# Kernel optimization log

Measured on AMD Instinct MI355X. Metric: run time of the kernel, lower is better.

## Reference

```python
import jax, jax.numpy as jnp
import numpy as np
from jax import lax

B, C, H, W = 64, 1, 256, 256
N = H * W
K = 16384  # positive_trials
LOG_CLAMP = -100.0  # torch BCELoss clamps log terms at -100


def setup_inputs() -> dict:
    key = jax.random.key(0)
    k1, k2, k3 = jax.random.split(key, 3)
    decision_scores = jax.random.normal(k1, (B, N, 2), dtype=jnp.float32)
    s_map = jax.random.uniform(k2, (B, C, H, W), dtype=jnp.float32)
    # gumbel noise g = -log(-log(U)), matching F.gumbel_softmax sampling
    u = jax.random.uniform(k3, (B, N, 2), dtype=jnp.float32, minval=1e-10, maxval=1.0)
    gumbel_noise = -jnp.log(-jnp.log(u))
    return {"decision_scores": decision_scores, "s_map": s_map, "gumbel_noise": gumbel_noise}


def reference(decision_scores, s_map, gumbel_noise):
    # Tokenizer: b c h w -> b (h w) c
    tokens = jnp.transpose(s_map.reshape(B, C, H * W), (0, 2, 1))  # [B, N, 1]
    # soft gumbel-softmax (tau=1, hard=False), keep prob of class 0
    soft = jax.nn.softmax(decision_scores + gumbel_noise, axis=-1)[:, :, 0:1]  # [B, N, 1]
    # top-K salient token indices per sample (descending sort -> top_k)
    _, idx = lax.top_k(tokens[:, :, 0], K)  # [B, K]
    trials = jnp.zeros((B, N), dtype=tokens.dtype)
    trials = trials.at[jnp.arange(B)[:, None], idx].set(1.0)[:, :, None]  # [B, N, 1]
    # BCE with reduction='sum', log clamped at -100 like torch
    log_p = jnp.clip(jnp.log(soft), LOG_CLAMP, None)
    log_1mp = jnp.clip(jnp.log(1.0 - soft), LOG_CLAMP, None)
    loss = -jnp.sum(trials * log_p + (1.0 - trials) * log_1mp)
    return loss
```

## Files before the change

### kernel.cpp

```cpp
#include <hip/hip_runtime.h>
#include <cstdint>

#define BATCH 64
#define NPIX 65536
#define TOPK 16384
#define NB 256
#define SEGS 32
#define WLO 186
#define WHI 198
#define NWBIN (WHI - WLO + 1)
#define CAPB 192
#define NSLOT (SEGS * CAPB)
#define FCAP 1024

__device__ __forceinline__ float block_reduce(float acc) {
    __shared__ float w[4];
    __syncthreads();
    #pragma unroll
    for (int off = 32; off > 0; off >>= 1) acc += __shfl_down(acc, off, 64);
    if ((threadIdx.x & 63) == 0) w[threadIdx.x >> 6] = acc;
    __syncthreads();
    return w[0] + w[1] + w[2] + w[3];
}

__device__ __forceinline__ float block_reduce1k(float acc) {
    __shared__ float w[16];
    __syncthreads();
    #pragma unroll
    for (int off = 32; off > 0; off >>= 1) acc += __shfl_down(acc, off, 64);
    if ((threadIdx.x & 63) == 0) w[threadIdx.x >> 6] = acc;
    __syncthreads();
    float s = 0.f;
    #pragma unroll
    for (int i = 0; i < 16; ++i) s += w[i];
    return s;
}

__device__ __forceinline__ void bce_from_d(float d, float& lp, float& llp) {
    float t = __logf(1.f + __expf(-fabsf(d)));
    lp  = fmaxf(fminf(d, 0.f) - t, -100.f);
    llp = fmaxf(-fmaxf(d, 0.f) - t, -100.f);
}

__device__ __forceinline__ int vkey(float v) {
    return (int)fminf(v * 256.0f, 255.0f);
}

__global__ __launch_bounds__(256) void k1_pass(
    const float4* __restrict__ sc, const float4* __restrict__ gn,
    const float2* __restrict__ tokp,
    float* __restrict__ pk1, float* __restrict__ psel, float* __restrict__ phi,
    uint32_t* __restrict__ gcc,
    uint32_t* __restrict__ cvb, uint32_t* __restrict__ cvi,
    uint32_t* __restrict__ cvd, float* __restrict__ out)
{
    __shared__ uint32_t bvb[CAPB], bvi[CAPB], bvd[CAPB];
    __shared__ uint32_t ccount;
    const int tid = threadIdx.x;
    if (tid < CAPB) { bvb[tid] = 0u; bvi[tid] = 0u; bvd[tid] = 0u; }
    if (tid == 0) { ccount = 0u; if (blockIdx.x == 0) out[0] = 0.f; }
    __syncthreads();

    const int b   = blockIdx.x >> 5;
    const int seg = blockIdx.x & (SEGS - 1);
    const int pairbase = b * (NPIX / 2) + seg * 1024;
    float acc = 0.f, asel = 0.f, chi = 0.f;

    #pragma unroll
    for (int it = 0; it < 4; ++it) {
        int j = pairbase + it * 256 + tid;
        float4 s = sc[j];
        float4 g = gn[j];
        float2 tk = tokp[j];
        int px0 = (j - b * (NPIX / 2)) * 2;
        {
            float d = (s.x + g.x) - (s.y + g.y);
            float lp, llp; bce_from_d(d, lp, llp);
            acc += llp;
            float diff = lp - llp;
            int k = vkey(tk.x);
            if (k > WHI) { asel += diff; chi += 1.f; }
            else if (k >= WLO) {
                uint32_t p = atomicAdd(&ccount, 1u);
                if (p < CAPB) {
                    bvb[p] = __float_as_uint(tk.x);
                    bvi[p] = (uint32_t)px0;
                    bvd[p] = __float_as_uint(diff);
                }
            }
        }
        {
            float d = (s.z + g.z) - (s.w + g.w);
            float lp, llp; bce_from_d(d, lp, llp);
            acc += llp;
            float diff = lp - llp;
            int k = vkey(tk.y);
            if (k > WHI) { asel += diff; chi += 1.f; }
            else if (k >= WLO) {
                uint32_t p = atomicAdd(&ccount, 1u);
                if (p < CAPB) {
                    bvb[p] = __float_as_uint(tk.y);
                    bvi[p] = (uint32_t)(px0 + 1);
                    bvd[p] = __float_as_uint(diff);
                }
            }
        }
    }
    __syncthreads();
    const size_t cbase = (size_t)blockIdx.x * CAPB;
    if (tid < CAPB) {
        cvb[cbase + tid] = bvb[tid];
        cvi[cbase + tid] = bvi[tid];
        cvd[cbase + tid] = bvd[tid];
    }
    if (tid == 0) gcc[blockIdx.x] = ccount;

    float t1 = block_reduce(acc);
    float t2 = block_reduce(asel);
    float t3 = block_reduce(chi);
    if (tid == 0) {
        pk1[blockIdx.x]  = t1;
        psel[blockIdx.x] = t2;
        phi[blockIdx.x]  = t3;
    }
}

__global__ __launch_bounds__(1024) void k4_finalize(
    const uint32_t* __restrict__ cvb, const uint32_t* __restrict__ cvi,
    const uint32_t* __restrict__ cvd, const uint32_t* __restrict__ gcc,
    const float* __restrict__ pk1, const float* __restrict__ psel,
    const float* __restrict__ phi,
    const float4* __restrict__ tok4,
    const float2* __restrict__ sc2, const float2* __restrict__ gn2,
    float* __restrict__ out)
{
    __shared__ uint32_t fvb[FCAP], fvi[FCAP];
    __shared__ float    fdf[FCAP];
    __shared__ uint32_t fh[NB];
    __shared__ uint32_t wlds[16 * NWBIN];
    __shared__ uint32_t wc[NWBIN];
    __shared__ uint32_t fcnt;
    __shared__ int      sh_sb, sh_ovf;
    __shared__ uint32_t sh_rem;

    const int b = blockIdx.x, tid = threadIdx.x;
    const int wave = tid >> 6, lane = tid & 63;
    if (tid == 0) { fcnt = 0u; sh_sb = -1; sh_ovf = 0; sh_rem = 1u; }
    __syncthreads();

    const size_t base = (size_t)b * NSLOT;

    int bc[NWBIN];
    #pragma unroll
    for (int i = 0; i < NWBIN; ++i) bc[i] = 0;
    #pragma unroll
    for (int it = 0; it < NSLOT / 1024; ++it) {
        int k = vkey(__uint_as_float(cvb[base + it * 1024 + tid]));
        #pragma unroll
        for (int i = 0; i < NWBIN; ++i) bc[i] += (k == WLO + i);
    }
    #pragma unroll
    for (int i = 0; i < NWBIN; ++i) {
        int v = bc[i];
        #pragma unroll
        for (int off = 32; off > 0; off >>= 1) v += __shfl_down(v, off, 64);
        if (lane == 0) wlds[wave * NWBIN + i] = (uint32_t)v;
    }
    if (tid < SEGS && gcc[b * SEGS + tid] > CAPB) sh_ovf = 1;
    __syncthreads();
    if (tid < NWBIN) {
        uint32_t u = 0;
        #pragma unroll
        for (int wv = 0; wv < 16; ++wv) u += wlds[wv * NWBIN + tid];
        wc[tid] = u;
    }
    float chl = (tid < SEGS) ? phi[b * SEGS + tid] : 0.f;
    float chf = block_reduce1k(chl);
    if (tid == 0) {
        uint32_t cnt_hi = (uint32_t)(chf + 0.5f);
        if (cnt_hi >= TOPK) sh_ovf = 1;
        else {
            uint32_t cum = cnt_hi;
            int found = -1; uint32_t rem = 1u;
            for (int jj = WHI; jj >= WLO; --jj) {
                uint32_t nc = cum + wc[jj - WLO];
                if (nc >= TOPK) { found = jj; rem = TOPK - cum; break; }
                cum = nc;
            }
            if (found < 0) sh_ovf = 1;
            else { sh_sb = found; sh_rem = rem; }
        }
    }
    __syncthreads();

    bool fast = (sh_ovf == 0);
    const int sb = sh_sb;
    float fac = (tid < SEGS) ? pk1[b * SEGS + tid] : 0.f;

    if (fast) {
        if (tid < SEGS) fac += psel[b * SEGS + tid];
        #pragma unroll
        for (int it = 0; it < NSLOT / 1024; ++it) {
            int t = it * 1024 + tid;
            uint32_t vb = cvb[base + t];
            int k = vkey(__uint_as_float(vb));
            if (k > sb) fac += __uint_as_float(cvd[base + t]);
            else if (k == sb) {
                uint32_t p = atomicAdd(&fcnt, 1u);
                if (p < FCAP) {
                    fvb[p] = vb;
                    fvi[p] = cvi[base + t] & (NPIX - 1);
                    fdf[p] = __uint_as_float(cvd[base + t]);
                }
            }
        }
        __syncthreads();
        if (fcnt > FCAP) fast = false;
        if (fast) {
            const uint32_t cnt = fcnt, rem = sh_rem;
            for (uint32_t j = tid; j < cnt; j += 1024) {
                const uint32_t mb = fvb[j], mi = fvi[j];
                uint32_t rank = 0;
                for (uint32_t i = 0; i < cnt; ++i) {
                    uint32_t ob = fvb[i];
                    rank += (ob > mb) || (ob == mb && fvi[i] < mi);
                }
                if (rank < rem) fac += fdf[j];
            }
        }
    }

    if (!fast) {
        fac = (tid < SEGS) ? pk1[b * SEGS + tid] : 0.f;
        for (int i = tid; i < NB; i += 1024) fh[i] = 0u;
        if (tid == 0) fcnt = 0u;
        __syncthreads();
        const float4* tbase = tok4 + (size_t)b * (NPIX / 4);
        for (int it = 0; it < NPIX / 4 / 1024; ++it) {
            float4 v = tbase[it * 1024 + tid];
            atomicAdd(&fh[vkey(v.x)], 1u);
            atomicAdd(&fh[vkey(v.y)], 1u);
            atomicAdd(&fh[vkey(v.z)], 1u);
            atomicAdd(&fh[vkey(v.w)], 1u);
        }
        __syncthreads();
        if (tid == 0) {
            uint32_t cum = 0; int bin = NB - 1;
            for (; bin > 0; --bin) {
                if (cum + fh[bin] >= TOPK) break;
                cum += fh[bin];
            }
            sh_sb = bin; sh_rem = TOPK - cum;
        }
        __syncthreads();
        const int sb2 = sh_sb; const uint32_t rem2 = sh_rem;
        for (int it = 0; it < NPIX / 4 / 1024; ++it) {
            int j = it * 1024 + tid;
            float4 v = tbase[j];
            int px = j * 4;
            float fv[4] = {v.x, v.y, v.z, v.w};
            #pragma unroll
            for (int q = 0; q < 4; ++q) {
                int k = vkey(fv[q]);
                if (k > sb2) {
                    size_t idx = (size_t)b * NPIX + (px + q);
                    float2 S = sc2[idx]; float2 G = gn2[idx];
                    float d = (S.x + G.x) - (S.y + G.y);
                    float lp, llp; bce_from_d(d, lp, llp);
                    fac += lp - llp;
                } else if (k == sb2) {
                    uint32_t p = atomicAdd(&fcnt, 1u);
                    if (p < FCAP) { fvb[p] = __float_as_uint(fv[q]); fvi[p] = (uint32_t)(px + q); }
                }
            }
        }
        __syncthreads();
        const uint32_t cnt2 = min(fcnt, (uint32_t)FCAP);
        for (uint32_t j = tid; j < cnt2; j += 1024) {
            const uint32_t mb = fvb[j], mi = fvi[j];
            uint32_t rank = 0;
            for (uint32_t i = 0; i < cnt2; ++i) {
                uint32_t ob = fvb[i];
                rank += (ob > mb) || (ob == mb && fvi[i] < mi);
            }
            if (rank < rem2) {
                size_t idx = (size_t)b * NPIX + (mi & (NPIX - 1));
                float2 S = sc2[idx]; float2 G = gn2[idx];
                float d = (S.x + G.x) - (S.y + G.y);
                float lp, llp; bce_from_d(d, lp, llp);
                fac += lp - llp;
            }
        }
    }

    float tot = block_reduce1k(fac);
    if (tid == 0) atomicAdd(out, -tot);
}

extern "C" void kernel_launch(void* const* d_in, const int* in_sizes, int n_in,
                              void* d_out, int out_size, void* d_ws, size_t ws_size,
                              hipStream_t stream) {
    const float* scores = (const float*)d_in[0];
    const float* smap   = (const float*)d_in[1];
    const float* gumbel = (const float*)d_in[2];
    float* out = (float*)d_out;

    char* ws = (char*)d_ws;
    float*    pk1  = (float*)ws;     ws += (size_t)BATCH * SEGS * 4;
    float*    psel = (float*)ws;     ws += (size_t)BATCH * SEGS * 4;
    float*    phi  = (float*)ws;     ws += (size_t)BATCH * SEGS * 4;
    uint32_t* gcc  = (uint32_t*)ws;  ws += (size_t)BATCH * SEGS * 4;
    uint32_t* cvb  = (uint32_t*)ws;  ws += (size_t)BATCH * NSLOT * 4;
    uint32_t* cvi  = (uint32_t*)ws;  ws += (size_t)BATCH * NSLOT * 4;
    uint32_t* cvd  = (uint32_t*)ws;  ws += (size_t)BATCH * NSLOT * 4;

    k1_pass<<<BATCH * SEGS, 256, 0, stream>>>(
        (const float4*)scores, (const float4*)gumbel, (const float2*)smap,
        pk1, psel, phi, gcc, cvb, cvi, cvd, out);

    k4_finalize<<<BATCH, 1024, 0, stream>>>(
        cvb, cvi, cvd, gcc, pk1, psel, phi,
        (const float4*)smap, (const float2*)scores, (const float2*)gumbel, out);
}
```

Measured before the change: 122.2 us.

## Fuse finalize into main pass via last-block-per-batch ticket and per-block window histograms

Merges the per-batch finalize kernel into the main pass: each block atomically takes a ticket on a per-batch counter, and the last of the 32 segment blocks for a batch runs the top-k threshold selection and BCE correction. Each block now builds a small LDS histogram of its candidate window bins and writes it out, so the finalizer sums 32 small histograms instead of rescanning all candidate slots. A tiny init kernel resets the counters and the output. This removes a kernel launch boundary and the tail of a 64-block finalize launch, but the finalizer now runs with 256 threads instead of 1024, and the larger LDS footprint may reduce occupancy for the main pass.

Measured after the change: 334.7 us. +173.9%, slower.

```diff
diff --git a/kernel.cpp b/kernel.cpp
--- a/kernel.cpp
+++ b/kernel.cpp
@@ -12,6 +12,7 @@
 #define CAPB 192
 #define NSLOT (SEGS * CAPB)
 #define FCAP 1024
+#define WHSTRIDE 16
 
 __device__ __forceinline__ float block_reduce(float acc) {
     __shared__ float w[4];
@@ -21,19 +22,6 @@
     if ((threadIdx.x & 63) == 0) w[threadIdx.x >> 6] = acc;
     __syncthreads();
     return w[0] + w[1] + w[2] + w[3];
-}
-
-__device__ __forceinline__ float block_reduce1k(float acc) {
-    __shared__ float w[16];
-    __syncthreads();
-    #pragma unroll
-    for (int off = 32; off > 0; off >>= 1) acc += __shfl_down(acc, off, 64);
-    if ((threadIdx.x & 63) == 0) w[threadIdx.x >> 6] = acc;
-    __syncthreads();
-    float s = 0.f;
-    #pragma unroll
-    for (int i = 0; i < 16; ++i) s += w[i];
-    return s;
 }
 
 __device__ __forceinline__ void bce_from_d(float d, float& lp, float& llp) {
@@ -46,19 +34,39 @@
     return (int)fminf(v * 256.0f, 255.0f);
 }
 
-__global__ __launch_bounds__(256) void k1_pass(
+__global__ void k0_init(uint32_t* __restrict__ bdone, float* __restrict__ out) {
+    if (threadIdx.x < BATCH) bdone[threadIdx.x] = 0u;
+    if (threadIdx.x == 0) out[0] = 0.f;
+}
+
+__global__ __launch_bounds__(256, 4) void k1_fused(
     const float4* __restrict__ sc, const float4* __restrict__ gn,
     const float2* __restrict__ tokp,
     float* __restrict__ pk1, float* __restrict__ psel, float* __restrict__ phi,
     uint32_t* __restrict__ gcc,
     uint32_t* __restrict__ cvb, uint32_t* __restrict__ cvi,
-    uint32_t* __restrict__ cvd, float* __restrict__ out)
+    uint32_t* __restrict__ cvd,
+    uint32_t* __restrict__ whist, uint32_t* __restrict__ bdone,
+    const float4* __restrict__ tok4,
+    const float2* __restrict__ sc2, const float2* __restrict__ gn2,
+    float* __restrict__ out)
 {
     __shared__ uint32_t bvb[CAPB], bvi[CAPB], bvd[CAPB];
+    __shared__ uint32_t sh_wh[NWBIN];
     __shared__ uint32_t ccount;
+    __shared__ uint32_t sh_ticket;
+    __shared__ uint32_t fvb[FCAP], fvi[FCAP];
+    __shared__ float    fdf[FCAP];
+    __shared__ uint32_t fh[NB];
+    __shared__ uint32_t wc[NWBIN];
+    __shared__ uint32_t fcnt;
+    __shared__ int      sh_sb, sh_ovf;
+    __shared__ uint32_t sh_rem;
+
     const int tid = threadIdx.x;
     if (tid < CAPB) { bvb[tid] = 0u; bvi[tid] = 0u; bvd[tid] = 0u; }
-    if (tid == 0) { ccount = 0u; if (blockIdx.x == 0) out[0] = 0.f; }
+    if (tid < NWBIN) sh_wh[tid] = 0u;
+    if (tid == 0) ccount = 0u;
     __syncthreads();
 
     const int b   = blockIdx.x >> 5;
@@ -107,13 +115,21 @@
         }
     }
     __syncthreads();
+    const uint32_t cc = ccount;
+    {
+        uint32_t nsl = cc < CAPB ? cc : CAPB;
+        if (tid < nsl) {
+            int k = vkey(__uint_as_float(bvb[tid]));
+            atomicAdd(&sh_wh[k - WLO], 1u);
+        }
+    }
     const size_t cbase = (size_t)blockIdx.x * CAPB;
     if (tid < CAPB) {
         cvb[cbase + tid] = bvb[tid];
         cvi[cbase + tid] = bvi[tid];
         cvd[cbase + tid] = bvd[tid];
     }
-    if (tid == 0) gcc[blockIdx.x] = ccount;
+    if (tid == 0) gcc[blockIdx.x] = cc;
 
     float t1 = block_reduce(acc);
     float t2 = block_reduce(asel);
@@ -123,59 +139,29 @@
         psel[blockIdx.x] = t2;
         phi[blockIdx.x]  = t3;
     }
-}
-
-__global__ __launch_bounds__(1024) void k4_finalize(
-    const uint32_t* __restrict__ cvb, const uint32_t* __restrict__ cvi,
-    const uint32_t* __restrict__ cvd, const uint32_t* __restrict__ gcc,
-    const float* __restrict__ pk1, const float* __restrict__ psel,
-    const float* __restrict__ phi,
-    const float4* __restrict__ tok4,
-    const float2* __restrict__ sc2, const float2* __restrict__ gn2,
-    float* __restrict__ out)
-{
-    __shared__ uint32_t fvb[FCAP], fvi[FCAP];
-    __shared__ float    fdf[FCAP];
-    __shared__ uint32_t fh[NB];
-    __shared__ uint32_t wlds[16 * NWBIN];
-    __shared__ uint32_t wc[NWBIN];
-    __shared__ uint32_t fcnt;
-    __shared__ int      sh_sb, sh_ovf;
-    __shared__ uint32_t sh_rem;
-
-    const int b = blockIdx.x, tid = threadIdx.x;
-    const int wave = tid >> 6, lane = tid & 63;
+    if (tid < NWBIN) whist[(size_t)blockIdx.x * WHSTRIDE + tid] = sh_wh[tid];
+
+    __threadfence();
+    __syncthreads();
+    if (tid == 0) sh_ticket = atomicAdd(&bdone[b], 1u);
+    __syncthreads();
+    if (sh_ticket != SEGS - 1) return;
+
+    __threadfence();
+
     if (tid == 0) { fcnt = 0u; sh_sb = -1; sh_ovf = 0; sh_rem = 1u; }
     __syncthreads();
 
-    const size_t base = (size_t)b * NSLOT;
-
-    int bc[NWBIN];
-    #pragma unroll
-    for (int i = 0; i < NWBIN; ++i) bc[i] = 0;
-    #pragma unroll
-    for (int it = 0; it < NSLOT / 1024; ++it) {
-        int k = vkey(__uint_as_float(cvb[base + it * 1024 + tid]));
-        #pragma unroll
-        for (int i = 0; i < NWBIN; ++i) bc[i] += (k == WLO + i);
-    }
-    #pragma unroll
-    for (int i = 0; i < NWBIN; ++i) {
-        int v = bc[i];
-        #pragma unroll
-        for (int off = 32; off > 0; off >>= 1) v += __shfl_down(v, off, 64);
-        if (lane == 0) wlds[wave * NWBIN + i] = (uint32_t)v;
-    }
     if (tid < SEGS && gcc[b * SEGS + tid] > CAPB) sh_ovf = 1;
-    __syncthreads();
     if (tid < NWBIN) {
         uint32_t u = 0;
         #pragma unroll
-        for (int wv = 0; wv < 16; ++wv) u += wlds[wv * NWBIN + tid];
+        for (int s = 0; s < SEGS; ++s)
+            u += whist[(size_t)(b * SEGS + s) * WHSTRIDE + tid];
         wc[tid] = u;
     }
     float chl = (tid < SEGS) ? phi[b * SEGS + tid] : 0.f;
-    float chf = block_reduce1k(chl);
+    float chf = block_reduce(chl);
     if (tid == 0) {
         uint32_t cnt_hi = (uint32_t)(chf + 0.5f);
         if (cnt_hi >= TOPK) sh_ovf = 1;
@@ -195,22 +181,24 @@
 
     bool fast = (sh_ovf == 0);
     const int sb = sh_sb;
+    const size_t fbase = (size_t)b * NSLOT;
     float fac = (tid < SEGS) ? pk1[b * SEGS + tid] : 0.f;
 
     if (fast) {
         if (tid < SEGS) fac += psel[b * SEGS + tid];
         #pragma unroll
-        for (int it = 0; it < NSLOT / 1024; ++it) {
-            int t = it * 1024 + tid;
-            uint32_t vb = cvb[base + t];
+        for (int it = 0; it < NSLOT / 256; ++it) {
+            int t = it * 256 + tid;
+            uint32_t vb = cvb[fbase + t];
+            uint32_t vd = cvd[fbase + t];
             int k = vkey(__uint_as_float(vb));
-            if (k > sb) fac += __uint_as_float(cvd[base + t]);
+            if (k > sb) fac += __uint_as_float(vd);
             else if (k == sb) {
                 uint32_t p = atomicAdd(&fcnt, 1u);
                 if (p < FCAP) {
                     fvb[p] = vb;
-                    fvi[p] = cvi[base + t] & (NPIX - 1);
-                    fdf[p] = __uint_as_float(cvd[base + t]);
+                    fvi[p] = cvi[fbase + t] & (NPIX - 1);
+                    fdf[p] = __uint_as_float(vd);
                 }
             }
         }
@@ -218,7 +206,7 @@
         if (fcnt > FCAP) fast = false;
         if (fast) {
             const uint32_t cnt = fcnt, rem = sh_rem;
-            for (uint32_t j = tid; j < cnt; j += 1024) {
+            for (uint32_t j = tid; j < cnt; j += 256) {
                 const uint32_t mb = fvb[j], mi = fvi[j];
                 uint32_t rank = 0;
                 for (uint32_t i = 0; i < cnt; ++i) {
@@ -232,12 +220,12 @@
 
     if (!fast) {
         fac = (tid < SEGS) ? pk1[b * SEGS + tid] : 0.f;
-        for (int i = tid; i < NB; i += 1024) fh[i] = 0u;
+        for (int i = tid; i < NB; i += 256) fh[i] = 0u;
         if (tid == 0) fcnt = 0u;
         __syncthreads();
         const float4* tbase = tok4 + (size_t)b * (NPIX / 4);
-        for (int it = 0; it < NPIX / 4 / 1024; ++it) {
-            float4 v = tbase[it * 1024 + tid];
+        for (int it = 0; it < NPIX / 4 / 256; ++it) {
+            float4 v = tbase[it * 256 + tid];
             atomicAdd(&fh[vkey(v.x)], 1u);
             atomicAdd(&fh[vkey(v.y)], 1u);
             atomicAdd(&fh[vkey(v.z)], 1u);
@@ -254,8 +242,8 @@
         }
         __syncthreads();
         const int sb2 = sh_sb; const uint32_t rem2 = sh_rem;
-        for (int it = 0; it < NPIX / 4 / 1024; ++it) {
-            int j = it * 1024 + tid;
+        for (int it = 0; it < NPIX / 4 / 256; ++it) {
+            int j = it * 256 + tid;
             float4 v = tbase[j];
             int px = j * 4;
             float fv[4] = {v.x, v.y, v.z, v.w};
@@ -276,7 +264,7 @@
         }
         __syncthreads();
         const uint32_t cnt2 = min(fcnt, (uint32_t)FCAP);
-        for (uint32_t j = tid; j < cnt2; j += 1024) {
+        for (uint32_t j = tid; j < cnt2; j += 256) {
             const uint32_t mb = fvb[j], mi = fvi[j];
             uint32_t rank = 0;
             for (uint32_t i = 0; i < cnt2; ++i) {
@@ -293,7 +281,7 @@
         }
     }
 
-    float tot = block_reduce1k(fac);
+    float tot = block_reduce(fac);
     if (tid == 0) atomicAdd(out, -tot);
 }
 
@@ -306,19 +294,20 @@
     float* out = (float*)d_out;
 
     char* ws = (char*)d_ws;
-    float*    pk1  = (float*)ws;     ws += (size_t)BATCH * SEGS * 4;
-    float*    psel = (float*)ws;     ws += (size_t)BATCH * SEGS * 4;
-    float*    phi  = (float*)ws;     ws += (size_t)BATCH * SEGS * 4;
-    uint32_t* gcc  = (uint32_t*)ws;  ws += (size_t)BATCH * SEGS * 4;
-    uint32_t* cvb  = (uint32_t*)ws;  ws += (size_t)BATCH * NSLOT * 4;
-    uint32_t* cvi  = (uint32_t*)ws;  ws += (size_t)BATCH * NSLOT * 4;
-    uint32_t* cvd  = (uint32_t*)ws;  ws += (size_t)BATCH * NSLOT * 4;
-
-    k1_pass<<<BATCH * SEGS, 256, 0, stream>>>(
+    float*    pk1   = (float*)ws;    ws += (size_t)BATCH * SEGS * 4;
+    float*    psel  = (float*)ws;    ws += (size_t)BATCH * SEGS * 4;
+    float*    phi   = (float*)ws;    ws += (size_t)BATCH * SEGS * 4;
+    uint32_t* gcc   = (uint32_t*)ws; ws += (size_t)BATCH * SEGS * 4;
+    uint32_t* cvb   = (uint32_t*)ws; ws += (size_t)BATCH * NSLOT * 4;
+    uint32_t* cvi   = (uint32_t*)ws; ws += (size_t)BATCH * NSLOT * 4;
+    uint32_t* cvd   = (uint32_t*)ws; ws += (size_t)BATCH * NSLOT * 4;
+    uint32_t* whist = (uint32_t*)ws; ws += (size_t)BATCH * SEGS * WHSTRIDE * 4;
+    uint32_t* bdone = (uint32_t*)ws; ws += (size_t)BATCH * 4;
+
+    k0_init<<<1, 64, 0, stream>>>(bdone, out);
+
+    k1_fused<<<BATCH * SEGS, 256, 0, stream>>>(
         (const float4*)scores, (const float4*)gumbel, (const float2*)smap,
-        pk1, psel, phi, gcc, cvb, cvi, cvd, out);
-
-    k4_finalize<<<BATCH, 1024, 0, stream>>>(
-        cvb, cvi, cvd, gcc, pk1, psel, phi,
+        pk1, psel, phi, gcc, cvb, cvi, cvd, whist, bdone,
         (const float4*)smap, (const float2*)scores, (const float2*)gumbel, out);
 }
```
